# Kernel tuning notes

Hardware: AMD Instinct MI355X
Metric: run time of the kernel (lower is better)

## Reference

```python
import jax, jax.numpy as jnp
import numpy as np

B, S, D_IN, D_H = 8, 4096, 256, 512
EPS = 1e-6


def setup_inputs() -> dict:
    key = jax.random.key(0)
    ks = jax.random.split(key, 5)
    scale = 1.0 / np.sqrt(D_IN)  # torch Linear default init scale (uniform bound)
    x = jax.random.normal(ks[0], (B, S, D_IN), dtype=jnp.float32)
    Wi = jax.random.normal(ks[1], (D_IN, D_H), dtype=jnp.float32) * scale
    Wf = jax.random.normal(ks[2], (D_IN, D_H), dtype=jnp.float32) * scale
    Wo = jax.random.normal(ks[3], (D_IN, D_H), dtype=jnp.float32) * scale
    Wz = jax.random.normal(ks[4], (D_IN, D_H), dtype=jnp.float32) * scale
    zb = jnp.zeros((D_H,), dtype=jnp.float32)
    return {"x": x, "Wi": Wi, "bi": zb, "Wf": Wf, "bf": zb,
            "Wo": Wo, "bo": zb, "Wz": Wz, "bz": zb}


def _xlstm_forward(x, Wi, bi, Wf, bf, Wo, bo, Wz, bz):
    # Batched projections over all timesteps at once: [B,S,D_H] each.
    i_t = jnp.exp(jnp.clip(jnp.einsum('bsd,dh->bsh', x, Wi) + bi, -20.0, 0.0))
    f_t = jnp.exp(jnp.clip(jnp.einsum('bsd,dh->bsh', x, Wf) + bf, -20.0, 0.0))
    o_t = jax.nn.sigmoid(jnp.einsum('bsd,dh->bsh', x, Wo) + bo)
    z_t = jnp.tanh(jnp.einsum('bsd,dh->bsh', x, Wz) + bz)

    def step(carry, gates):
        c, n = carry
        i, f, o, z = gates
        c = f * c + i * z
        n = f * n + i
        h = o * (c / (n + EPS))
        return (c, n), h

    c0 = jnp.zeros((x.shape[0], Wi.shape[1]), dtype=x.dtype)
    n0 = jnp.ones((x.shape[0], Wi.shape[1]), dtype=x.dtype)
    # time-major scan over the recurrence
    gates_tm = tuple(jnp.swapaxes(g, 0, 1) for g in (i_t, f_t, o_t, z_t))  # [S,B,H]
    _, h_tm = jax.lax.scan(step, (c0, n0), gates_tm)
    return jnp.swapaxes(h_tm, 0, 1)  # [B,S,H]


def reference(x, Wi, bi, Wf, bf, Wo, bo, Wz, bz):
    return _xlstm_forward(x, Wi, bi, Wf, bf, Wo, bo, Wz, bz)
```

## Files before the change

kernel.cpp:

```cpp
#include <hip/hip_runtime.h>
#include <hip/hip_bf16.h>
#include <cstdint>
#include <cstddef>

typedef __hip_bfloat16 bf16;
typedef __attribute__((ext_vector_type(8))) short short8;
typedef __attribute__((ext_vector_type(4))) short short4v;
typedef __attribute__((ext_vector_type(4))) float floatx4;

#define BB 8
#define SS 4096
#define DIN 256
#define DH 512
#define NCH 128
#define CHUNK 32

__device__ __forceinline__ float b2f(bf16 v) { return __bfloat162float(v); }
__device__ __forceinline__ float sh2f(short v) {
    unsigned int u = ((unsigned int)(unsigned short)v) << 16;
    float f; __builtin_memcpy(&f, &u, 4); return f;
}
__device__ __forceinline__ float frcp(float x) { return __builtin_amdgcn_rcpf(x); }

__global__ __launch_bounds__(256) void convert_x(
    const float* __restrict__ X, bf16* __restrict__ Xb)
{
    const int idx = blockIdx.x * 256 + threadIdx.x;
    float4 v = ((const float4*)X)[idx];
    bf16 o[4] = {__float2bfloat16(v.x), __float2bfloat16(v.y),
                 __float2bfloat16(v.z), __float2bfloat16(v.w)};
    ((short4v*)Xb)[idx] = *(const short4v*)o;
}

__global__ __launch_bounds__(256) void transpose_w(
    const float* __restrict__ Wi, const float* __restrict__ Wf,
    const float* __restrict__ Wo, const float* __restrict__ Wz,
    bf16* __restrict__ Wt)
{
    int o  = blockIdx.x * 256 + threadIdx.x;
    int nf = o >> 8;
    int k  = o & 255;
    int g  = nf >> 9;
    int hh = nf & 511;
    const float* W = (g == 0) ? Wi : (g == 1) ? Wf : (g == 2) ? Wo : Wz;
    Wt[o] = __float2bfloat16(W[(size_t)k * DH + hh]);
}

__device__ __forceinline__ void load16_lds(const bf16* g, short* l)
{
    __builtin_amdgcn_global_load_lds(
        (const __attribute__((address_space(1))) unsigned int*)g,
        (__attribute__((address_space(3))) unsigned int*)l,
        16, 0, 0);
}

__global__ __launch_bounds__(256) void gemm_mfma(
    const bf16* __restrict__ Xb, const bf16* __restrict__ Wt,
    const float* __restrict__ bi, const float* __restrict__ bfv,
    const float* __restrict__ bo, const float* __restrict__ bz,
    bf16* __restrict__ Pi, bf16* __restrict__ Pf,
    bf16* __restrict__ Po, bf16* __restrict__ Pz)
{
    __shared__ __align__(16) short As[128 * 32];
    __shared__ __align__(16) short Bs[128 * 32];

    const int tid  = threadIdx.x;
    const int m0   = blockIdx.x * 128;
    const int n0   = blockIdx.y * 128;
    const int wave = tid >> 6, lane = tid & 63;
    const int wm   = (wave >> 1) * 64, wn = (wave & 1) * 64;
    const int l15  = lane & 15;
    const int q    = lane >> 4;

    floatx4 acc[4][4];
#pragma unroll
    for (int i = 0; i < 4; i++)
#pragma unroll
        for (int j = 0; j < 4; j++) acc[i][j] = (floatx4){0.f, 0.f, 0.f, 0.f};

    const int r_ld = tid >> 2;
    const int c_ld = tid & 3;
    const bf16* agp0 = Xb + (size_t)(m0 + r_ld) * DIN + c_ld * 8;
    const bf16* agp1 = Xb + (size_t)(m0 + 64 + r_ld) * DIN + c_ld * 8;
    const bf16* bgp0 = Wt + (size_t)(n0 + r_ld) * DIN + c_ld * 8;
    const bf16* bgp1 = Wt + (size_t)(n0 + 64 + r_ld) * DIN + c_ld * 8;

    for (int k0 = 0; k0 < DIN; k0 += 32) {
        load16_lds(agp0 + k0, &As[tid * 8]);
        load16_lds(agp1 + k0, &As[2048 + tid * 8]);
        load16_lds(bgp0 + k0, &Bs[tid * 8]);
        load16_lds(bgp1 + k0, &Bs[2048 + tid * 8]);
        __syncthreads();

        short8 af[4], bfr[4];
#pragma unroll
        for (int ti = 0; ti < 4; ti++)
            af[ti] = *(const short8*)&As[(wm + ti * 16 + l15) * 32 + q * 8];
#pragma unroll
        for (int tj = 0; tj < 4; tj++)
            bfr[tj] = *(const short8*)&Bs[(wn + tj * 16 + l15) * 32 + q * 8];
#pragma unroll
        for (int ti = 0; ti < 4; ti++)
#pragma unroll
            for (int tj = 0; tj < 4; tj++)
                acc[ti][tj] = __builtin_amdgcn_mfma_f32_16x16x32_bf16(
                    af[ti], bfr[tj], acc[ti][tj], 0, 0, 0);
        __syncthreads();
    }

    const int g = n0 >> 9;
    const float* bias = (g == 0) ? bi : (g == 1) ? bfv : (g == 2) ? bo : bz;
    bf16* pb = (g == 0) ? Pi : (g == 1) ? Pf : (g == 2) ? Po : Pz;

#pragma unroll
    for (int ti = 0; ti < 4; ti++) {
        const int mrow = m0 + wm + ti * 16 + q * 4;
#pragma unroll
        for (int tj = 0; tj < 4; tj++) {
            const int hh = (n0 + wn + tj * 16 + l15) & 511;
            const float bsv = bias[hh];
#pragma unroll
            for (int r = 0; r < 4; r++) {
                const float v = acc[ti][tj][r] + bsv;
                float a;
                if (g == 0 || g == 1) {
                    a = __expf(fminf(fmaxf(v, -20.f), 0.f));
                } else if (g == 2) {
                    a = frcp(1.f + __expf(-v));
                } else {
                    a = 1.f - 2.f * frcp(__expf(2.f * v) + 1.f);
                }
                pb[(size_t)(mrow + r) * DH + hh] = __float2bfloat16(a);
            }
        }
    }
}

__global__ __launch_bounds__(256) void scan_carry(
    const bf16* __restrict__ Pi, const bf16* __restrict__ Pf,
    const bf16* __restrict__ Pz,
    float* __restrict__ Aa, float* __restrict__ Bca, float* __restrict__ Bna,
    int nb)
{
    const int tid = threadIdx.x;
    const int ch  = blockIdx.x * 4 + (tid >> 6);
    const int b   = blockIdx.y;
    const int hg  = (tid & 63) * 8;
    const size_t base = ((size_t)(b * SS + ch * CHUNK)) * DH + hg;

    float A[8], Bc[8], Bn[8];
#pragma unroll
    for (int j = 0; j < 8; j++) { A[j] = 1.f; Bc[j] = 0.f; Bn[j] = 0.f; }

#pragma unroll 4
    for (int s = 0; s < CHUNK; s++) {
        const size_t o = base + (size_t)s * DH;
        short8 i8 = *(const short8*)(Pi + o);
        short8 f8 = *(const short8*)(Pf + o);
        short8 z8 = *(const short8*)(Pz + o);
#pragma unroll
        for (int j = 0; j < 8; j++) {
            const float f  = sh2f(f8[j]);
            const float iv = sh2f(i8[j]);
            const float zv = sh2f(z8[j]);
            Bc[j] = fmaf(f, Bc[j], iv * zv);
            Bn[j] = fmaf(f, Bn[j], iv);
            A[j] *= f;
        }
    }
    const size_t cidx = (size_t)(ch * nb + b) * DH + hg;
#pragma unroll
    for (int j = 0; j < 2; j++) {
        *(floatx4*)(Aa  + cidx + j * 4) = *(floatx4*)&A[j * 4];
        *(floatx4*)(Bca + cidx + j * 4) = *(floatx4*)&Bc[j * 4];
        *(floatx4*)(Bna + cidx + j * 4) = *(floatx4*)&Bn[j * 4];
    }
}

__global__ __launch_bounds__(256) void scan_chunks(
    const float* __restrict__ Aa, const float* __restrict__ Bca,
    const float* __restrict__ Bna,
    float* __restrict__ Cs, float* __restrict__ Ns, int nb)
{
    const int t = blockIdx.x * 256 + threadIdx.x;
    float c = 0.f, n = 1.f;
    for (int ch = 0; ch < NCH; ch++) {
        const size_t cidx = (size_t)ch * (nb * DH) + t;
        Cs[cidx] = c; Ns[cidx] = n;
        const float A = Aa[cidx];
        c = fmaf(A, c, Bca[cidx]);
        n = fmaf(A, n, Bna[cidx]);
    }
}

__global__ __launch_bounds__(256) void scan_emit(
    const bf16* __restrict__ Pi, const bf16* __restrict__ Pf,
    const bf16* __restrict__ Po, const bf16* __restrict__ Pz,
    const float* __restrict__ Cs, const float* __restrict__ Ns,
    float* __restrict__ out, int nb)
{
    const int tid = threadIdx.x;
    const int ch  = blockIdx.x * 4 + (tid >> 6);
    const int b   = blockIdx.y;
    const int hg  = (tid & 63) * 8;
    const size_t base = ((size_t)(b * SS + ch * CHUNK)) * DH + hg;
    const size_t cidx = (size_t)(ch * nb + b) * DH + hg;

    float c[8], n[8];
#pragma unroll
    for (int j = 0; j < 2; j++) {
        *(floatx4*)&c[j * 4] = *(const floatx4*)(Cs + cidx + j * 4);
        *(floatx4*)&n[j * 4] = *(const floatx4*)(Ns + cidx + j * 4);
    }

#pragma unroll 4
    for (int s = 0; s < CHUNK; s++) {
        const size_t o = base + (size_t)s * DH;
        short8 i8 = *(const short8*)(Pi + o);
        short8 f8 = *(const short8*)(Pf + o);
        short8 o8 = *(const short8*)(Po + o);
        short8 z8 = *(const short8*)(Pz + o);
        float h[8];
#pragma unroll
        for (int j = 0; j < 8; j++) {
            const float f  = sh2f(f8[j]);
            const float iv = sh2f(i8[j]);
            const float ov = sh2f(o8[j]);
            const float zv = sh2f(z8[j]);
            c[j] = fmaf(f, c[j], iv * zv);
            n[j] = fmaf(f, n[j], iv);
            h[j] = ov * c[j] * frcp(n[j] + 1e-6f);
        }
        *(floatx4*)(out + o)     = *(floatx4*)&h[0];
        *(floatx4*)(out + o + 4) = *(floatx4*)&h[4];
    }
}

extern "C" void kernel_launch(void* const* d_in, const int* in_sizes, int n_in,
                              void* d_out, int out_size, void* d_ws, size_t ws_size,
                              hipStream_t stream)
{
    const float* x   = (const float*)d_in[0];
    const float* Wi  = (const float*)d_in[1];
    const float* bi  = (const float*)d_in[2];
    const float* Wf  = (const float*)d_in[3];
    const float* bfv = (const float*)d_in[4];
    const float* Wo  = (const float*)d_in[5];
    const float* bo  = (const float*)d_in[6];
    const float* Wz  = (const float*)d_in[7];
    const float* bz  = (const float*)d_in[8];
    float* out = (float*)d_out;

    int nb = BB;
    while (nb > 1) {
        size_t need = (1u << 20)
                    + (size_t)nb * SS * DIN * 2
                    + 4 * (size_t)nb * SS * DH * 2
                    + 5 * (size_t)NCH * nb * DH * 4;
        if (need <= ws_size) break;
        nb >>= 1;
    }

    const size_t plane = (size_t)nb * SS * DH;
    bf16* Wt = (bf16*)d_ws;
    bf16* Xb = (bf16*)((char*)d_ws + (1u << 20));
    bf16* Pi = Xb + (size_t)nb * SS * DIN;
    bf16* Pf = Pi + plane;
    bf16* Po = Pf + plane;
    bf16* Pz = Po + plane;
    float* Aa  = (float*)(Pz + plane);
    float* Bca = Aa  + (size_t)NCH * nb * DH;
    float* Bna = Bca + (size_t)NCH * nb * DH;
    float* Cs  = Bna + (size_t)NCH * nb * DH;
    float* Ns  = Cs  + (size_t)NCH * nb * DH;

    transpose_w<<<2048, 256, 0, stream>>>(Wi, Wf, Wo, Wz, Wt);

    for (int b0 = 0; b0 < BB; b0 += nb) {
        const float* Xsrc = x   + (size_t)b0 * SS * DIN;
        float*       Ob   = out + (size_t)b0 * SS * DH;
        convert_x<<<nb * 1024, 256, 0, stream>>>(Xsrc, Xb);
        gemm_mfma<<<dim3(nb * SS / 128, 16), 256, 0, stream>>>(
            Xb, Wt, bi, bfv, bo, bz, Pi, Pf, Po, Pz);
        scan_carry<<<dim3(NCH / 4, nb), 256, 0, stream>>>(
            Pi, Pf, Pz, Aa, Bca, Bna, nb);
        scan_chunks<<<2 * nb, 256, 0, stream>>>(Aa, Bca, Bna, Cs, Ns, nb);
        scan_emit<<<dim3(NCH / 4, nb), 256, 0, stream>>>(
            Pi, Pf, Po, Pz, Cs, Ns, Ob, nb);
    }
}
```

Before: 244.6 us.

## Fuse per-chunk scan carry computation into GEMM epilogue via LDS-staged gates

The GEMM now tiles 64 timesteps by 64 hidden units and computes all four gates for that tile in one block, with one wave per gate. The activated gates are staged in LDS, written out coalesced, and reused to compute chunk carry products (A, Bc, Bn) directly. This removes the separate scan_carry kernel and its re-read of the Pi/Pf/Pz planes. In exchange the chunk size is halved to 16, which doubles the number of chunks handled by the sequential scan_chunks pass and by scan_emit, and the block now uses more LDS.

```diff
diff --git a/kernel.cpp b/kernel.cpp
--- a/kernel.cpp
+++ b/kernel.cpp
@@ -12,8 +12,8 @@
 #define SS 4096
 #define DIN 256
 #define DH 512
-#define NCH 128
-#define CHUNK 32
+#define NCH 256
+#define CHUNK 16
 
 __device__ __forceinline__ float b2f(bf16 v) { return __bfloat162float(v); }
 __device__ __forceinline__ float sh2f(short v) {
@@ -54,21 +54,23 @@
         16, 0, 0);
 }
 
-__global__ __launch_bounds__(256) void gemm_mfma(
+__global__ __launch_bounds__(256) void gemm_fused(
     const bf16* __restrict__ Xb, const bf16* __restrict__ Wt,
     const float* __restrict__ bi, const float* __restrict__ bfv,
     const float* __restrict__ bo, const float* __restrict__ bz,
     bf16* __restrict__ Pi, bf16* __restrict__ Pf,
-    bf16* __restrict__ Po, bf16* __restrict__ Pz)
-{
-    __shared__ __align__(16) short As[128 * 32];
-    __shared__ __align__(16) short Bs[128 * 32];
+    bf16* __restrict__ Po, bf16* __restrict__ Pz,
+    float* __restrict__ Aa, float* __restrict__ Bca, float* __restrict__ Bna,
+    int nb)
+{
+    __shared__ __align__(16) short As[64 * 32];
+    __shared__ __align__(16) short Bs[256 * 32];
+    __shared__ __align__(16) bf16  Gb[4 * 64 * 64];
 
     const int tid  = threadIdx.x;
-    const int m0   = blockIdx.x * 128;
-    const int n0   = blockIdx.y * 128;
+    const int m0   = blockIdx.x * 64;
+    const int h0   = blockIdx.y * 64;
     const int wave = tid >> 6, lane = tid & 63;
-    const int wm   = (wave >> 1) * 64, wn = (wave & 1) * 64;
     const int l15  = lane & 15;
     const int q    = lane >> 4;
 
@@ -78,27 +80,29 @@
 #pragma unroll
         for (int j = 0; j < 4; j++) acc[i][j] = (floatx4){0.f, 0.f, 0.f, 0.f};
 
-    const int r_ld = tid >> 2;
-    const int c_ld = tid & 3;
-    const bf16* agp0 = Xb + (size_t)(m0 + r_ld) * DIN + c_ld * 8;
-    const bf16* agp1 = Xb + (size_t)(m0 + 64 + r_ld) * DIN + c_ld * 8;
-    const bf16* bgp0 = Wt + (size_t)(n0 + r_ld) * DIN + c_ld * 8;
-    const bf16* bgp1 = Wt + (size_t)(n0 + 64 + r_ld) * DIN + c_ld * 8;
+    const int rr = tid >> 2;
+    const int cc = (tid & 3) * 8;
+    const bf16* agp = Xb + (size_t)(m0 + rr) * DIN + cc;
+    const bf16* bgp0 = Wt + (size_t)(0 * 512 + h0 + rr) * DIN + cc;
+    const bf16* bgp1 = Wt + (size_t)(1 * 512 + h0 + rr) * DIN + cc;
+    const bf16* bgp2 = Wt + (size_t)(2 * 512 + h0 + rr) * DIN + cc;
+    const bf16* bgp3 = Wt + (size_t)(3 * 512 + h0 + rr) * DIN + cc;
 
     for (int k0 = 0; k0 < DIN; k0 += 32) {
-        load16_lds(agp0 + k0, &As[tid * 8]);
-        load16_lds(agp1 + k0, &As[2048 + tid * 8]);
-        load16_lds(bgp0 + k0, &Bs[tid * 8]);
-        load16_lds(bgp1 + k0, &Bs[2048 + tid * 8]);
+        load16_lds(agp + k0, &As[tid * 8]);
+        load16_lds(bgp0 + k0, &Bs[0 * 2048 + tid * 8]);
+        load16_lds(bgp1 + k0, &Bs[1 * 2048 + tid * 8]);
+        load16_lds(bgp2 + k0, &Bs[2 * 2048 + tid * 8]);
+        load16_lds(bgp3 + k0, &Bs[3 * 2048 + tid * 8]);
         __syncthreads();
 
         short8 af[4], bfr[4];
 #pragma unroll
         for (int ti = 0; ti < 4; ti++)
-            af[ti] = *(const short8*)&As[(wm + ti * 16 + l15) * 32 + q * 8];
+            af[ti] = *(const short8*)&As[(ti * 16 + l15) * 32 + q * 8];
 #pragma unroll
         for (int tj = 0; tj < 4; tj++)
-            bfr[tj] = *(const short8*)&Bs[(wn + tj * 16 + l15) * 32 + q * 8];
+            bfr[tj] = *(const short8*)&Bs[wave * 2048 + (tj * 16 + l15) * 32 + q * 8];
 #pragma unroll
         for (int ti = 0; ti < 4; ti++)
 #pragma unroll
@@ -108,72 +112,63 @@
         __syncthreads();
     }
 
-    const int g = n0 >> 9;
-    const float* bias = (g == 0) ? bi : (g == 1) ? bfv : (g == 2) ? bo : bz;
-    bf16* pb = (g == 0) ? Pi : (g == 1) ? Pf : (g == 2) ? Po : Pz;
-
+    const float* bias = (wave == 0) ? bi : (wave == 1) ? bfv
+                      : (wave == 2) ? bo : bz;
+    bf16* gb = &Gb[wave * 4096];
 #pragma unroll
     for (int ti = 0; ti < 4; ti++) {
-        const int mrow = m0 + wm + ti * 16 + q * 4;
 #pragma unroll
         for (int tj = 0; tj < 4; tj++) {
-            const int hh = (n0 + wn + tj * 16 + l15) & 511;
-            const float bsv = bias[hh];
+            const int h = tj * 16 + l15;
+            const float bsv = bias[h0 + h];
 #pragma unroll
             for (int r = 0; r < 4; r++) {
+                const int s = ti * 16 + q * 4 + r;
                 const float v = acc[ti][tj][r] + bsv;
                 float a;
-                if (g == 0 || g == 1) {
+                if (wave == 0 || wave == 1)
                     a = __expf(fminf(fmaxf(v, -20.f), 0.f));
-                } else if (g == 2) {
+                else if (wave == 2)
                     a = frcp(1.f + __expf(-v));
-                } else {
+                else
                     a = 1.f - 2.f * frcp(__expf(2.f * v) + 1.f);
-                }
-                pb[(size_t)(mrow + r) * DH + hh] = __float2bfloat16(a);
+                gb[s * 64 + h] = __float2bfloat16(a);
             }
         }
     }
-}
-
-__global__ __launch_bounds__(256) void scan_carry(
-    const bf16* __restrict__ Pi, const bf16* __restrict__ Pf,
-    const bf16* __restrict__ Pz,
-    float* __restrict__ Aa, float* __restrict__ Bca, float* __restrict__ Bna,
-    int nb)
-{
-    const int tid = threadIdx.x;
-    const int ch  = blockIdx.x * 4 + (tid >> 6);
-    const int b   = blockIdx.y;
-    const int hg  = (tid & 63) * 8;
-    const size_t base = ((size_t)(b * SS + ch * CHUNK)) * DH + hg;
-
-    float A[8], Bc[8], Bn[8];
-#pragma unroll
-    for (int j = 0; j < 8; j++) { A[j] = 1.f; Bc[j] = 0.f; Bn[j] = 0.f; }
-
-#pragma unroll 4
-    for (int s = 0; s < CHUNK; s++) {
-        const size_t o = base + (size_t)s * DH;
-        short8 i8 = *(const short8*)(Pi + o);
-        short8 f8 = *(const short8*)(Pf + o);
-        short8 z8 = *(const short8*)(Pz + o);
-#pragma unroll
-        for (int j = 0; j < 8; j++) {
-            const float f  = sh2f(f8[j]);
-            const float iv = sh2f(i8[j]);
-            const float zv = sh2f(z8[j]);
-            Bc[j] = fmaf(f, Bc[j], iv * zv);
-            Bn[j] = fmaf(f, Bn[j], iv);
-            A[j] *= f;
+    __syncthreads();
+
+    bf16* const planes[4] = {Pi, Pf, Po, Pz};
+#pragma unroll
+    for (int p = 0; p < 8; p++) {
+        const int cid = p * 256 + tid;
+        const int g   = cid >> 9;
+        const int rem = cid & 511;
+        const int s   = rem >> 3;
+        const int c   = rem & 7;
+        short8 v8 = *(const short8*)&Gb[g * 4096 + s * 64 + c * 8];
+        *(short8*)&planes[g][(size_t)(m0 + s) * DH + h0 + c * 8] = v8;
+    }
+
+    {
+        const int hh  = tid & 63;
+        const int sub = tid >> 6;
+        float A = 1.f, Bc = 0.f, Bn = 0.f;
+#pragma unroll
+        for (int s = 0; s < CHUNK; s++) {
+            const int sl = sub * CHUNK + s;
+            const float f  = b2f(Gb[1 * 4096 + sl * 64 + hh]);
+            const float iv = b2f(Gb[0 * 4096 + sl * 64 + hh]);
+            const float zv = b2f(Gb[3 * 4096 + sl * 64 + hh]);
+            Bc = fmaf(f, Bc, iv * zv);
+            Bn = fmaf(f, Bn, iv);
+            A *= f;
         }
-    }
-    const size_t cidx = (size_t)(ch * nb + b) * DH + hg;
-#pragma unroll
-    for (int j = 0; j < 2; j++) {
-        *(floatx4*)(Aa  + cidx + j * 4) = *(floatx4*)&A[j * 4];
-        *(floatx4*)(Bca + cidx + j * 4) = *(floatx4*)&Bc[j * 4];
-        *(floatx4*)(Bna + cidx + j * 4) = *(floatx4*)&Bn[j * 4];
+        const int b  = m0 >> 12;
+        const int s0 = m0 & (SS - 1);
+        const int ch = (s0 >> 4) + sub;
+        const size_t cidx = ((size_t)ch * nb + b) * DH + h0 + hh;
+        Aa[cidx] = A; Bca[cidx] = Bc; Bna[cidx] = Bn;
     }
 }
 
@@ -280,10 +275,8 @@
         const float* Xsrc = x   + (size_t)b0 * SS * DIN;
         float*       Ob   = out + (size_t)b0 * SS * DH;
         convert_x<<<nb * 1024, 256, 0, stream>>>(Xsrc, Xb);
-        gemm_mfma<<<dim3(nb * SS / 128, 16), 256, 0, stream>>>(
-            Xb, Wt, bi, bfv, bo, bz, Pi, Pf, Po, Pz);
-        scan_carry<<<dim3(NCH / 4, nb), 256, 0, stream>>>(
-            Pi, Pf, Pz, Aa, Bca, Bna, nb);
+        gemm_fused<<<dim3(nb * SS / 64, DH / 64), 256, 0, stream>>>(
+            Xb, Wt, bi, bfv, bo, bz, Pi, Pf, Po, Pz, Aa, Bca, Bna, nb);
         scan_chunks<<<2 * nb, 256, 0, stream>>>(Aa, Bca, Bna, Cs, Ns, nb);
         scan_emit<<<dim3(NCH / 4, nb), 256, 0, stream>>>(
             Pi, Pf, Po, Pz, Cs, Ns, Ob, nb);
```

Measured after the change: 253.3 us. 3.6% more time.
